# Optimization experiments

Measured on AMD Instinct MI355X. Metric: run time of the kernel, lower is better.

## Reference

```python
import jax, jax.numpy as jnp
import numpy as np

N_NODES = 100000
N_EDGES = 1600000
D_IN = 64
D_HID = 64
D_OUT = 64
DROP_P = 0.5


def _degree_norms(src, dst, n):
    ones = jnp.ones(src.shape[0], dtype=jnp.float32)
    deg_out = jax.ops.segment_sum(ones, src, num_segments=n)  # out-degree of src nodes
    deg_in = jax.ops.segment_sum(ones, dst, num_segments=n)   # in-degree of dst nodes
    norm_src = jnp.where(deg_out > 0, jax.lax.rsqrt(jnp.maximum(deg_out, 1.0)), 0.0)
    norm_dst = jnp.where(deg_in > 0, jax.lax.rsqrt(jnp.maximum(deg_in, 1.0)), 0.0)
    return norm_src, norm_dst


def _graph_conv(h, W, b, src, dst, norm_src, norm_dst, n, activation=None):
    # DGL GraphConv, norm='both': out = D_in^{-1/2} A (D_out^{-1/2} h) W + b
    h = h * norm_src[:, None]
    h = h @ W                      # small GEMM first (in >= out), math-equivalent
    msg = h[src]                   # gather  [E, d]
    agg = jax.ops.segment_sum(msg, dst, num_segments=n)  # scatter-add [N, d]
    out = agg * norm_dst[:, None] + b
    if activation is not None:
        out = activation(out)
    return out


def _dropout(h, key, p=DROP_P):
    keep = jax.random.bernoulli(key, 1.0 - p, h.shape)
    return jnp.where(keep, h / (1.0 - p), 0.0)


def setup_inputs() -> dict:
    key = jax.random.key(0)
    ks = jax.random.split(key, 6)
    x = jax.random.normal(ks[0], (N_NODES, D_IN), dtype=jnp.float32)
    W0 = jax.random.normal(ks[1], (D_IN, D_HID), dtype=jnp.float32) * 0.05
    W1 = jax.random.normal(ks[2], (D_HID, D_HID), dtype=jnp.float32) * 0.05
    W2 = jax.random.normal(ks[3], (D_HID, D_OUT), dtype=jnp.float32) * 0.05
    b0 = jnp.zeros((D_HID,), dtype=jnp.float32)
    b1 = jnp.zeros((D_HID,), dtype=jnp.float32)
    b2 = jnp.zeros((D_OUT,), dtype=jnp.float32)
    src = jax.random.randint(ks[4], (N_EDGES,), 0, N_NODES, dtype=jnp.int32)
    dst = jax.random.randint(ks[5], (N_EDGES,), 0, N_NODES, dtype=jnp.int32)
    return {"x": x, "W0": W0, "b0": b0, "W1": W1, "b1": b1, "W2": W2, "b2": b2,
            "src": src, "dst": dst}


def reference(x, W0, b0, W1, b1, W2, b2, src, dst):
    n = x.shape[0]
    norm_src, norm_dst = _degree_norms(src, dst, n)
    dk = jax.random.key(1)
    h = _graph_conv(x, W0, b0, src, dst, norm_src, norm_dst, n, jax.nn.relu)
    h = _dropout(h, jax.random.fold_in(dk, 0))
    h = _graph_conv(h, W1, b1, src, dst, norm_src, norm_dst, n, jax.nn.relu)
    h = _dropout(h, jax.random.fold_in(dk, 1))
    h = _graph_conv(h, W2, b2, src, dst, norm_src, norm_dst, n, None)
    return h
```

## Files before the change

kernel.cpp:

```cpp
#include <hip/hip_runtime.h>
#include <hip/hip_bf16.h>
#include <hip/hip_fp16.h>
#include <cstddef>


#define WG 256
#define WGD 1024
#define SLOT_S 48
#define NB_SHIFT 9
#define NB_W 512
#define EB 2048
#define PSTRIDE 257

__host__ __device__ static inline unsigned rotl32(unsigned x, int r) {
  return (x << r) | (x >> (32 - r));
}

__host__ __device__ static inline void threefry2x32(unsigned k0, unsigned k1,
                                                    unsigned x0, unsigned x1,
                                                    unsigned& o0, unsigned& o1) {
  unsigned ks2 = k0 ^ k1 ^ 0x1BD11BDAu;
  x0 += k0; x1 += k1;
#define TF_ROUND(r) { x0 += x1; x1 = rotl32(x1, r); x1 ^= x0; }
  TF_ROUND(13) TF_ROUND(15) TF_ROUND(26) TF_ROUND(6)
  x0 += k1;  x1 += ks2 + 1u;
  TF_ROUND(17) TF_ROUND(29) TF_ROUND(16) TF_ROUND(24)
  x0 += ks2; x1 += k0 + 2u;
  TF_ROUND(13) TF_ROUND(15) TF_ROUND(26) TF_ROUND(6)
  x0 += k0;  x1 += k1 + 3u;
  TF_ROUND(17) TF_ROUND(29) TF_ROUND(16) TF_ROUND(24)
  x0 += k1;  x1 += ks2 + 4u;
  TF_ROUND(13) TF_ROUND(15) TF_ROUND(26) TF_ROUND(6)
  x0 += ks2; x1 += k0 + 5u;
#undef TF_ROUND
  o0 = x0; o1 = x1;
}

__device__ static inline float2 h2f(unsigned u) {
  return __half22float2(__builtin_bit_cast(__half2, u));
}
__device__ static inline unsigned f2h(float a, float b) {
  return __builtin_bit_cast(unsigned, __floats2half2_rn(a, b));
}


__global__ __launch_bounds__(WG) void bin_k(
    const int* __restrict__ src, const int* __restrict__ dst,
    unsigned* __restrict__ binbuf_d, unsigned short* __restrict__ binbuf_s,
    unsigned short* __restrict__ pref_d, unsigned short* __restrict__ pref_s,
    int e) {
  __shared__ int hist_d[256], hist_s[256];
  __shared__ int scan_d[256], scan_s[256];
  __shared__ int curs_d[256], curs_s[256];
  __shared__ unsigned sorted_d[EB];
  __shared__ unsigned short sorted_s[EB];
  int tid = threadIdx.x;
  int blk = blockIdx.x;
  int base = blk * EB;
  int cnt = e - base;
  if (cnt > EB) cnt = EB;

  hist_d[tid] = 0;
  hist_s[tid] = 0;
  __syncthreads();
  for (int i = tid; i < cnt; i += WG) {
    int d = dst[base + i];
    int s = src[base + i];
    atomicAdd(&hist_d[d >> NB_SHIFT], 1);
    atomicAdd(&hist_s[s >> NB_SHIFT], 1);
  }
  __syncthreads();
  int hd = hist_d[tid], hs = hist_s[tid];
  scan_d[tid] = hd;
  scan_s[tid] = hs;
  __syncthreads();
  for (int st = 1; st < 256; st <<= 1) {
    int ad = (tid >= st) ? scan_d[tid - st] : 0;
    int as = (tid >= st) ? scan_s[tid - st] : 0;
    __syncthreads();
    scan_d[tid] += ad;
    scan_s[tid] += as;
    __syncthreads();
  }
  int ed = scan_d[tid] - hd;
  int es = scan_s[tid] - hs;
  curs_d[tid] = ed;
  curs_s[tid] = es;
  pref_d[(size_t)blk * PSTRIDE + tid] = (unsigned short)ed;
  pref_s[(size_t)blk * PSTRIDE + tid] = (unsigned short)es;
  if (tid == 255) {
    pref_d[(size_t)blk * PSTRIDE + 256] = (unsigned short)scan_d[255];
    pref_s[(size_t)blk * PSTRIDE + 256] = (unsigned short)scan_s[255];
  }
  __syncthreads();
  for (int i = tid; i < cnt; i += WG) {
    int d = dst[base + i];
    int s = src[base + i];
    int pd = atomicAdd(&curs_d[d >> NB_SHIFT], 1);
    sorted_d[pd] = ((unsigned)(d & (NB_W - 1)) << 17) | (unsigned)s;
    int ps = atomicAdd(&curs_s[s >> NB_SHIFT], 1);
    sorted_s[ps] = (unsigned short)(s & (NB_W - 1));
  }
  __syncthreads();
  for (int i = tid; i < cnt; i += WG) binbuf_d[base + i] = sorted_d[i];
  for (int i = tid; i < cnt; i += WG) binbuf_s[base + i] = sorted_s[i];
}


__global__ __launch_bounds__(WGD) void debin_k(
    const unsigned* __restrict__ binbuf_d,
    const unsigned short* __restrict__ binbuf_s,
    const unsigned short* __restrict__ pref_d,
    const unsigned short* __restrict__ pref_s,
    int* __restrict__ slot, int* __restrict__ cnt_in,
    float* __restrict__ nsrc, const float* __restrict__ x,
    unsigned short* __restrict__ G0, int n, int nblk, int nbuck) {
  __shared__ int lcnt[NB_W];
  __shared__ float lns[NB_W];
  int tid = threadIdx.x;
  int b = blockIdx.x;
  for (int i = tid; i < NB_W; i += WGD) lcnt[i] = 0;
  __syncthreads();
  if (b < nbuck) {
    for (int seg = tid; seg < nblk; seg += WGD) {
      const unsigned short* pr = pref_d + (size_t)seg * PSTRIDE + b;
      int p0 = pr[0], p1 = pr[1];
      const unsigned* bb = binbuf_d + (size_t)seg * EB;
      for (int i = p0; i < p1; ++i) {
        unsigned v = bb[i];
        int dl = v >> 17;
        int s = (int)(v & 0x1FFFFu);
        int c = atomicAdd(&lcnt[dl], 1);
        if (c < SLOT_S) slot[(size_t)((b << NB_SHIFT) + dl) * SLOT_S + c] = s;
      }
    }
    __syncthreads();
    for (int i = tid; i < NB_W; i += WGD) {
      int v = (b << NB_SHIFT) + i;
      if (v < n) cnt_in[v] = lcnt[i];
    }
  } else {
    int b2 = b - nbuck;
    for (int seg = tid; seg < nblk; seg += WGD) {
      const unsigned short* pr = pref_s + (size_t)seg * PSTRIDE + b2;
      int p0 = pr[0], p1 = pr[1];
      const unsigned short* bb = binbuf_s + (size_t)seg * EB;
      for (int i = p0; i < p1; ++i) atomicAdd(&lcnt[bb[i]], 1);
    }
    __syncthreads();
    int vbase = b2 << NB_SHIFT;
    for (int i = tid; i < NB_W; i += WGD) {
      int v = vbase + i;
      if (v < n) {
        int c = lcnt[i];
        float ns = (c > 0) ? rsqrtf((float)c) : 0.f;
        lns[i] = ns;
        nsrc[v] = ns;
      }
    }
    __syncthreads();
    const float4* x4 = (const float4*)x;
    uint2* G2 = (uint2*)G0;
    int lim = NB_W * 16;
    for (int idx = tid; idx < lim; idx += WGD) {
      int nl = idx >> 4;
      int v = vbase + nl;
      if (v < n) {
        float ns = lns[nl];
        float4 r = x4[(size_t)v * 16 + (idx & 15)];
        G2[(size_t)v * 16 + (idx & 15)] =
            make_uint2(f2h(r.x * ns, r.y * ns), f2h(r.z * ns, r.w * ns));
      }
    }
  }
}

__global__ __launch_bounds__(WG) void layer_k(
    const unsigned short* __restrict__ G, const int* __restrict__ slot,
    const int* __restrict__ cnt_in, const float* __restrict__ nsrc,
    const float* __restrict__ W, const float* __restrict__ bias,
    unsigned short* __restrict__ GoutH, float* __restrict__ GoutF,
    int n, int mid, unsigned dk0, unsigned dk1) {
  __shared__ float4 Ws[1024];
  __shared__ __align__(16) float rows[4][272];
  const float4* W4 = (const float4*)W;
  for (int i = threadIdx.x; i < 1024; i += WG) Ws[i] = W4[i];

  int wave = threadIdx.x >> 6;
  int lane = threadIdx.x & 63;
  int g = lane >> 4;
  int l16 = lane & 15;
  int v = blockIdx.x * 16 + wave * 4 + g;
  bool valid = (v < n);
  int vc = valid ? v : (n - 1);

  int degt = valid ? cnt_in[vc] : 0;
  int deg = (degt > SLOT_S) ? SLOT_S : degt;
  const int* sl = slot + (size_t)vc * SLOT_S;
  const uint2* G2 = (const uint2*)G;

  float4 aA = make_float4(0.f, 0.f, 0.f, 0.f);
  float4 aB = make_float4(0.f, 0.f, 0.f, 0.f);
  float4 aC = make_float4(0.f, 0.f, 0.f, 0.f);
  float4 aD = make_float4(0.f, 0.f, 0.f, 0.f);
#define ACC(dst, m) { float2 lo = h2f((m).x), hi = h2f((m).y); \
    dst.x += lo.x; dst.y += lo.y; dst.z += hi.x; dst.w += hi.y; }
  int nq = deg >> 2;
  int i = 0;
  for (; i + 1 < nq; i += 2) {
    int4 q0 = *(const int4*)(sl + i * 4);
    int4 q1 = *(const int4*)(sl + i * 4 + 4);
    uint2 m0 = G2[(size_t)q0.x * 16 + l16];
    uint2 m1 = G2[(size_t)q0.y * 16 + l16];
    uint2 m2 = G2[(size_t)q0.z * 16 + l16];
    uint2 m3 = G2[(size_t)q0.w * 16 + l16];
    uint2 m4 = G2[(size_t)q1.x * 16 + l16];
    uint2 m5 = G2[(size_t)q1.y * 16 + l16];
    uint2 m6 = G2[(size_t)q1.z * 16 + l16];
    uint2 m7 = G2[(size_t)q1.w * 16 + l16];
    ACC(aA, m0) ACC(aB, m1) ACC(aC, m2) ACC(aD, m3)
    ACC(aA, m4) ACC(aB, m5) ACC(aC, m6) ACC(aD, m7)
  }
  if (i < nq) {
    int4 q0 = *(const int4*)(sl + i * 4);
    uint2 m0 = G2[(size_t)q0.x * 16 + l16];
    uint2 m1 = G2[(size_t)q0.y * 16 + l16];
    uint2 m2 = G2[(size_t)q0.z * 16 + l16];
    uint2 m3 = G2[(size_t)q0.w * 16 + l16];
    ACC(aA, m0) ACC(aB, m1) ACC(aC, m2) ACC(aD, m3)
  }
  int rem = deg & 3;
  if (rem) {
    int4 q = *(const int4*)(sl + (deg & ~3));
    int s0 = q.x;
    int s1 = (rem > 1) ? q.y : s0;
    int s2 = (rem > 2) ? q.z : s0;
    float w1 = (rem > 1) ? 1.f : 0.f;
    float w2 = (rem > 2) ? 1.f : 0.f;
    uint2 m0 = G2[(size_t)s0 * 16 + l16];
    uint2 m1 = G2[(size_t)s1 * 16 + l16];
    uint2 m2 = G2[(size_t)s2 * 16 + l16];
    ACC(aA, m0)
    { float2 lo = h2f(m1.x), hi = h2f(m1.y);
      aB.x = fmaf(w1, lo.x, aB.x); aB.y = fmaf(w1, lo.y, aB.y);
      aB.z = fmaf(w1, hi.x, aB.z); aB.w = fmaf(w1, hi.y, aB.w); }
    { float2 lo = h2f(m2.x), hi = h2f(m2.y);
      aC.x = fmaf(w2, lo.x, aC.x); aC.y = fmaf(w2, lo.y, aC.y);
      aC.z = fmaf(w2, hi.x, aC.z); aC.w = fmaf(w2, hi.y, aC.w); }
  }
#undef ACC
  float4 agg;
  agg.x = (aA.x + aB.x) + (aC.x + aD.x);
  agg.y = (aA.y + aB.y) + (aC.y + aD.y);
  agg.z = (aA.z + aB.z) + (aC.z + aD.z);
  agg.w = (aA.w + aB.w) + (aC.w + aD.w);

  float* rw = &rows[wave][g * 68];
  *(float4*)(rw + l16 * 4) = agg;
  __syncthreads();

  float4 acc = make_float4(0.f, 0.f, 0.f, 0.f);
#pragma unroll
  for (int k = 0; k < 64; ++k) {
    float a = rw[k];
    float4 w = Ws[k * 16 + l16];
    acc.x = fmaf(a, w.x, acc.x);
    acc.y = fmaf(a, w.y, acc.y);
    acc.z = fmaf(a, w.z, acc.z);
    acc.w = fmaf(a, w.w, acc.w);
  }

  float nd = (degt > 0) ? rsqrtf((float)degt) : 0.f;
  float4 b4 = ((const float4*)bias)[l16];
  float4 o;
  o.x = fmaf(acc.x, nd, b4.x);
  o.y = fmaf(acc.y, nd, b4.y);
  o.z = fmaf(acc.z, nd, b4.z);
  o.w = fmaf(acc.w, nd, b4.w);
  if (mid) {
    o.x = fmaxf(o.x, 0.f); o.y = fmaxf(o.y, 0.f);
    o.z = fmaxf(o.z, 0.f); o.w = fmaxf(o.w, 0.f);
    unsigned idx = (unsigned)(v * 64 + l16 * 4);
    unsigned r0a, r0b, r1a, r1b, r2a, r2b, r3a, r3b;
    threefry2x32(dk0, dk1, 0u, idx + 0u, r0a, r0b);
    threefry2x32(dk0, dk1, 0u, idx + 1u, r1a, r1b);
    threefry2x32(dk0, dk1, 0u, idx + 2u, r2a, r2b);
    threefry2x32(dk0, dk1, 0u, idx + 3u, r3a, r3b);
    float ns2 = 2.f * nsrc[vc];
    o.x = ((r0a ^ r0b) & 0x80000000u) ? 0.f : o.x * ns2;
    o.y = ((r1a ^ r1b) & 0x80000000u) ? 0.f : o.y * ns2;
    o.z = ((r2a ^ r2b) & 0x80000000u) ? 0.f : o.z * ns2;
    o.w = ((r3a ^ r3b) & 0x80000000u) ? 0.f : o.w * ns2;
    if (valid)
      ((uint2*)GoutH)[(size_t)v * 16 + l16] =
          make_uint2(f2h(o.x, o.y), f2h(o.z, o.w));
  } else {
    if (valid) ((float4*)GoutF)[(size_t)v * 16 + l16] = o;
  }
}


extern "C" void kernel_launch(void* const* d_in, const int* in_sizes, int n_in,
                              void* d_out, int out_size, void* d_ws, size_t ws_size,
                              hipStream_t stream) {
  const float* x  = (const float*)d_in[0];
  const float* W0 = (const float*)d_in[1];
  const float* b0 = (const float*)d_in[2];
  const float* W1 = (const float*)d_in[3];
  const float* b1 = (const float*)d_in[4];
  const float* W2 = (const float*)d_in[5];
  const float* b2 = (const float*)d_in[6];
  const int* src  = (const int*)d_in[7];
  const int* dst  = (const int*)d_in[8];
  float* out = (float*)d_out;

  const int n = in_sizes[0] / 64;
  const int e = in_sizes[7];
  const int nbuck = (n + NB_W - 1) / NB_W;
  const int nblk = (e + EB - 1) / EB;

  char* w = (char*)d_ws;
  size_t off = 0;
  auto alloc = [&](size_t bytes) -> void* {
    void* p = w + off;
    off += (bytes + 255) & ~(size_t)255;
    return p;
  };
  int*            cnt_in   = (int*)alloc((size_t)n * 4);
  float*          nsrc     = (float*)alloc((size_t)n * 4);
  unsigned*       binbuf_d = (unsigned*)alloc((size_t)nblk * EB * 4);
  unsigned short* binbuf_s = (unsigned short*)alloc((size_t)nblk * EB * 2);
  unsigned short* pref_d   = (unsigned short*)alloc((size_t)nblk * PSTRIDE * 2);
  unsigned short* pref_s   = (unsigned short*)alloc((size_t)nblk * PSTRIDE * 2);
  int*            slot     = (int*)alloc((size_t)nbuck * NB_W * SLOT_S * 4);
  unsigned short* G0       = (unsigned short*)alloc((size_t)n * 64 * 2);
  unsigned short* G1       = (unsigned short*)alloc((size_t)n * 64 * 2);

  unsigned k0a, k0b, k1a, k1b;
  threefry2x32(0u, 1u, 0u, 0u, k0a, k0b);
  threefry2x32(0u, 1u, 0u, 1u, k1a, k1b);

  const int gL = (n + 15) / 16;

  bin_k<<<nblk, WG, 0, stream>>>(src, dst, binbuf_d, binbuf_s,
                                 pref_d, pref_s, e);
  debin_k<<<2 * nbuck, WGD, 0, stream>>>(binbuf_d, binbuf_s, pref_d, pref_s,
                                         slot, cnt_in, nsrc, x, G0,
                                         n, nblk, nbuck);

  layer_k<<<gL, WG, 0, stream>>>(G0, slot, cnt_in, nsrc, W0, b0, G1, nullptr,
                                 n, 1, k0a, k0b);
  layer_k<<<gL, WG, 0, stream>>>(G1, slot, cnt_in, nsrc, W1, b1, G0, nullptr,
                                 n, 1, k1a, k1b);
  layer_k<<<gL, WG, 0, stream>>>(G0, slot, cnt_in, nsrc, W2, b2, nullptr, out,
                                 n, 0, 0u, 0u);
}
```

Measured before the change: 289.1 us.

## Parallelize debin per wave, interleave bucket roles, split x scaling kernel

```diff
diff --git a/kernel.cpp b/kernel.cpp
--- a/kernel.cpp
+++ b/kernel.cpp
@@ -5,7 +5,9 @@
 
 
 #define WG 256
+#define WGB 512
 #define WGD 1024
+#define NWAVES (WGD / 64)
 #define SLOT_S 48
 #define NB_SHIFT 9
 #define NB_W 512
@@ -44,7 +46,7 @@
 }
 
 
-__global__ __launch_bounds__(WG) void bin_k(
+__global__ __launch_bounds__(WGB) void bin_k(
     const int* __restrict__ src, const int* __restrict__ dst,
     unsigned* __restrict__ binbuf_d, unsigned short* __restrict__ binbuf_s,
     unsigned short* __restrict__ pref_d, unsigned short* __restrict__ pref_s,
@@ -60,40 +62,43 @@
   int cnt = e - base;
   if (cnt > EB) cnt = EB;
 
-  hist_d[tid] = 0;
-  hist_s[tid] = 0;
-  __syncthreads();
-  for (int i = tid; i < cnt; i += WG) {
+  if (tid < 256) { hist_d[tid] = 0; hist_s[tid] = 0; }
+  __syncthreads();
+  for (int i = tid; i < cnt; i += WGB) {
     int d = dst[base + i];
     int s = src[base + i];
     atomicAdd(&hist_d[d >> NB_SHIFT], 1);
     atomicAdd(&hist_s[s >> NB_SHIFT], 1);
   }
   __syncthreads();
-  int hd = hist_d[tid], hs = hist_s[tid];
-  scan_d[tid] = hd;
-  scan_s[tid] = hs;
+  int hd = 0, hs = 0;
+  if (tid < 256) {
+    hd = hist_d[tid]; hs = hist_s[tid];
+    scan_d[tid] = hd;
+    scan_s[tid] = hs;
+  }
   __syncthreads();
   for (int st = 1; st < 256; st <<= 1) {
-    int ad = (tid >= st) ? scan_d[tid - st] : 0;
-    int as = (tid >= st) ? scan_s[tid - st] : 0;
+    int ad = 0, as = 0;
+    if (tid < 256 && tid >= st) { ad = scan_d[tid - st]; as = scan_s[tid - st]; }
     __syncthreads();
-    scan_d[tid] += ad;
-    scan_s[tid] += as;
+    if (tid < 256) { scan_d[tid] += ad; scan_s[tid] += as; }
     __syncthreads();
   }
-  int ed = scan_d[tid] - hd;
-  int es = scan_s[tid] - hs;
-  curs_d[tid] = ed;
-  curs_s[tid] = es;
-  pref_d[(size_t)blk * PSTRIDE + tid] = (unsigned short)ed;
-  pref_s[(size_t)blk * PSTRIDE + tid] = (unsigned short)es;
-  if (tid == 255) {
-    pref_d[(size_t)blk * PSTRIDE + 256] = (unsigned short)scan_d[255];
-    pref_s[(size_t)blk * PSTRIDE + 256] = (unsigned short)scan_s[255];
-  }
-  __syncthreads();
-  for (int i = tid; i < cnt; i += WG) {
+  if (tid < 256) {
+    int ed = scan_d[tid] - hd;
+    int es = scan_s[tid] - hs;
+    curs_d[tid] = ed;
+    curs_s[tid] = es;
+    pref_d[(size_t)blk * PSTRIDE + tid] = (unsigned short)ed;
+    pref_s[(size_t)blk * PSTRIDE + tid] = (unsigned short)es;
+    if (tid == 255) {
+      pref_d[(size_t)blk * PSTRIDE + 256] = (unsigned short)scan_d[255];
+      pref_s[(size_t)blk * PSTRIDE + 256] = (unsigned short)scan_s[255];
+    }
+  }
+  __syncthreads();
+  for (int i = tid; i < cnt; i += WGB) {
     int d = dst[base + i];
     int s = src[base + i];
     int pd = atomicAdd(&curs_d[d >> NB_SHIFT], 1);
@@ -102,8 +107,8 @@
     sorted_s[ps] = (unsigned short)(s & (NB_W - 1));
   }
   __syncthreads();
-  for (int i = tid; i < cnt; i += WG) binbuf_d[base + i] = sorted_d[i];
-  for (int i = tid; i < cnt; i += WG) binbuf_s[base + i] = sorted_s[i];
+  for (int i = tid; i < cnt; i += WGB) binbuf_d[base + i] = sorted_d[i];
+  for (int i = tid; i < cnt; i += WGB) binbuf_s[base + i] = sorted_s[i];
 }
 
 
@@ -113,20 +118,28 @@
     const unsigned short* __restrict__ pref_d,
     const unsigned short* __restrict__ pref_s,
     int* __restrict__ slot, int* __restrict__ cnt_in,
-    float* __restrict__ nsrc, const float* __restrict__ x,
-    unsigned short* __restrict__ G0, int n, int nblk, int nbuck) {
+    float* __restrict__ nsrc, int n, int nblk, int nwg) {
   __shared__ int lcnt[NB_W];
-  __shared__ float lns[NB_W];
   int tid = threadIdx.x;
-  int b = blockIdx.x;
+  int wave = tid >> 6;
+  int lane = tid & 63;
+
+  int j = blockIdx.x;
+  int q = nwg >> 3, r = nwg & 7;
+  int x = j & 7, p = j >> 3;
+  int vb = (x < r ? x * (q + 1) : r * (q + 1) + (x - r) * q) + p;
+  int role = vb & 1;
+  int b = vb >> 1;
+
   for (int i = tid; i < NB_W; i += WGD) lcnt[i] = 0;
   __syncthreads();
-  if (b < nbuck) {
-    for (int seg = tid; seg < nblk; seg += WGD) {
+
+  if (role == 0) {
+    for (int seg = wave; seg < nblk; seg += NWAVES) {
       const unsigned short* pr = pref_d + (size_t)seg * PSTRIDE + b;
       int p0 = pr[0], p1 = pr[1];
       const unsigned* bb = binbuf_d + (size_t)seg * EB;
-      for (int i = p0; i < p1; ++i) {
+      for (int i = p0 + lane; i < p1; i += 64) {
         unsigned v = bb[i];
         int dl = v >> 17;
         int s = (int)(v & 0x1FFFFu);
@@ -140,39 +153,35 @@
       if (v < n) cnt_in[v] = lcnt[i];
     }
   } else {
-    int b2 = b - nbuck;
-    for (int seg = tid; seg < nblk; seg += WGD) {
-      const unsigned short* pr = pref_s + (size_t)seg * PSTRIDE + b2;
+    for (int seg = wave; seg < nblk; seg += NWAVES) {
+      const unsigned short* pr = pref_s + (size_t)seg * PSTRIDE + b;
       int p0 = pr[0], p1 = pr[1];
       const unsigned short* bb = binbuf_s + (size_t)seg * EB;
-      for (int i = p0; i < p1; ++i) atomicAdd(&lcnt[bb[i]], 1);
+      for (int i = p0 + lane; i < p1; i += 64) atomicAdd(&lcnt[bb[i]], 1);
     }
     __syncthreads();
-    int vbase = b2 << NB_SHIFT;
+    int vbase = b << NB_SHIFT;
     for (int i = tid; i < NB_W; i += WGD) {
       int v = vbase + i;
       if (v < n) {
         int c = lcnt[i];
-        float ns = (c > 0) ? rsqrtf((float)c) : 0.f;
-        lns[i] = ns;
-        nsrc[v] = ns;
+        nsrc[v] = (c > 0) ? rsqrtf((float)c) : 0.f;
       }
     }
-    __syncthreads();
-    const float4* x4 = (const float4*)x;
-    uint2* G2 = (uint2*)G0;
-    int lim = NB_W * 16;
-    for (int idx = tid; idx < lim; idx += WGD) {
-      int nl = idx >> 4;
-      int v = vbase + nl;
-      if (v < n) {
-        float ns = lns[nl];
-        float4 r = x4[(size_t)v * 16 + (idx & 15)];
-        G2[(size_t)v * 16 + (idx & 15)] =
-            make_uint2(f2h(r.x * ns, r.y * ns), f2h(r.z * ns, r.w * ns));
-      }
-    }
-  }
+  }
+}
+
+
+__global__ __launch_bounds__(WG) void ns_k(
+    const float* __restrict__ nsrc, const float* __restrict__ x,
+    unsigned short* __restrict__ G0, int n) {
+  int idx = blockIdx.x * WG + threadIdx.x;
+  int v = idx >> 4;
+  if (v >= n) return;
+  float ns = nsrc[v];
+  float4 rr = ((const float4*)x)[(size_t)v * 16 + (idx & 15)];
+  ((uint2*)G0)[(size_t)v * 16 + (idx & 15)] =
+      make_uint2(f2h(rr.x * ns, rr.y * ns), f2h(rr.z * ns, rr.w * ns));
 }
 
 __global__ __launch_bounds__(WG) void layer_k(
@@ -341,12 +350,14 @@
   threefry2x32(0u, 1u, 0u, 1u, k1a, k1b);
 
   const int gL = (n + 15) / 16;
-
-  bin_k<<<nblk, WG, 0, stream>>>(src, dst, binbuf_d, binbuf_s,
-                                 pref_d, pref_s, e);
+  const int gN = (n * 16 + WG - 1) / WG;
+
+  bin_k<<<nblk, WGB, 0, stream>>>(src, dst, binbuf_d, binbuf_s,
+                                  pref_d, pref_s, e);
   debin_k<<<2 * nbuck, WGD, 0, stream>>>(binbuf_d, binbuf_s, pref_d, pref_s,
-                                         slot, cnt_in, nsrc, x, G0,
-                                         n, nblk, nbuck);
+                                         slot, cnt_in, nsrc, n, nblk,
+                                         2 * nbuck);
+  ns_k<<<gN, WG, 0, stream>>>(nsrc, x, G0, n);
 
   layer_k<<<gL, WG, 0, stream>>>(G0, slot, cnt_in, nsrc, W0, b0, G1, nullptr,
                                  n, 1, k0a, k0b);
```

New measurement: 280.4 us. 3.0% less time.
